# Performance work log

Hardware: AMD Instinct MI355X
Metric: run time of the kernel (lower is better)

The kernel has to match this reference:

```python
import jax, jax.numpy as jnp
import numpy as np

NODE_DIM, EDGE_DIM, HIDDEN = 64, 16, 128
B, N, E, EA = 4, 10000, 320000, 80000


def _lin(key, fan_in, fan_out):
    # xavier-uniform like torch init
    bound = (6.0 / (fan_in + fan_out)) ** 0.5
    w = jax.random.uniform(key, (fan_in, fan_out), jnp.float32, -bound, bound)
    b = jnp.zeros((fan_out,), jnp.float32)
    return w, b


def setup_inputs() -> dict:
    key = jax.random.key(0)
    ks = jax.random.split(key, 12)
    nodes = jax.random.normal(ks[0], (B, N, NODE_DIM), jnp.float32)
    edge_index = jax.random.randint(ks[1], (2, E), 0, N, jnp.int64)
    edge_attr = jax.random.normal(ks[2], (B, E, EDGE_DIM), jnp.float32)
    edge_type_mask = jax.random.randint(ks[3], (EA,), 0, E, jnp.int64)
    p = {}
    p['g1_mw1'], p['g1_mb1'] = _lin(ks[4], 2 * NODE_DIM + EDGE_DIM, HIDDEN)
    p['g1_mw2'], p['g1_mb2'] = _lin(ks[5], HIDDEN, HIDDEN)
    p['g1_uw'], p['g1_ub'] = _lin(ks[6], NODE_DIM + HIDDEN, HIDDEN)
    p['g2_mw1'], p['g2_mb1'] = _lin(ks[7], 2 * HIDDEN + EDGE_DIM, HIDDEN)
    p['g2_mw2'], p['g2_mb2'] = _lin(ks[8], HIDDEN, HIDDEN)
    p['g2_uw'], p['g2_ub'] = _lin(ks[9], HIDDEN + HIDDEN, HIDDEN)
    p['a_w1'], p['a_b1'] = _lin(ks[10], 2 * HIDDEN + EDGE_DIM, HIDDEN)
    p['a_w2'], p['a_b2'] = _lin(ks[11], HIDDEN, 2)
    return dict(nodes=nodes, edge_index=edge_index, edge_attr=edge_attr,
                edge_type_mask=edge_type_mask, **p)


def _gnn_layer(node_attr, edge_index, edge_attr, mw1, mb1, mw2, mb2, uw, ub):
    r, s = edge_index[0], edge_index[1]
    h_recv = node_attr[:, r, :]          # [B,E,D] gather
    h_sent = node_attr[:, s, :]
    msg_in = jnp.concatenate([h_recv, h_sent, edge_attr], axis=-1)
    msg = jax.nn.relu(msg_in @ mw1 + mb1) @ mw2 + mb2   # [B,E,H]
    Bn, Nn, _ = node_attr.shape
    agg = jnp.zeros((Bn, Nn, msg.shape[-1]), msg.dtype).at[:, r, :].add(msg)
    upd_in = jnp.concatenate([node_attr, agg], axis=-1)
    return jax.nn.relu(upd_in @ uw + ub)


def reference(nodes, edge_index, edge_attr, edge_type_mask,
              g1_mw1, g1_mb1, g1_mw2, g1_mb2, g1_uw, g1_ub,
              g2_mw1, g2_mb1, g2_mw2, g2_mb2, g2_uw, g2_ub,
              a_w1, a_b1, a_w2, a_b2):
    h = _gnn_layer(nodes, edge_index, edge_attr, g1_mw1, g1_mb1, g1_mw2, g1_mb2, g1_uw, g1_ub)
    h = _gnn_layer(h, edge_index, edge_attr, g2_mw1, g2_mb1, g2_mw2, g2_mb2, g2_uw, g2_ub)
    # actor head: gather active edges only
    r, s = edge_index[0], edge_index[1]
    ra, sa = r[edge_type_mask], s[edge_type_mask]
    h_recv_a = h[:, ra, :]
    h_sent_a = h[:, sa, :]
    e_a = edge_attr[:, edge_type_mask, :]
    x = jnp.concatenate([h_recv_a, h_sent_a, e_a], axis=-1)
    out = jax.nn.relu(x @ a_w1 + a_b1) @ a_w2 + a_b2     # [B,EA,2]
    out = out.reshape(out.shape[0], -1, 2, out.shape[2]).mean(axis=2)  # avg edge pairs
    mean = out[:, :, 0]
    log_std = jnp.clip(out[:, :, 1], -20.0, 2.0)
    std = jnp.exp(log_std)
    return mean, std
```

## Files before the change

### kernel.cpp

```cpp
#include <hip/hip_runtime.h>
#include <hip/hip_bf16.h>
#include <math.h>

constexpr int Bn  = 4;
constexpr int Nn  = 10000;
constexpr int En  = 320000;
constexpr int EAn = 80000;
constexpr int OUT_N = 2 * Bn * (EAn / 2);

__global__ __launch_bounds__(256) void fill_sentinel(float* out, float v) {
    const int i = blockIdx.x * 256 + threadIdx.x;
    if (i < OUT_N) out[i] = v;
}

__global__ __launch_bounds__(256) void decode_indices(const void* __restrict__ ei_raw,
                                                      const void* __restrict__ mask_raw,
                                                      int* __restrict__ ei32,
                                                      int* __restrict__ mask32) {
    __shared__ int is64;
    if (threadIdx.x == 0) {
        const long long* p = (const long long*)ei_raw;
        int ok = 1;
        for (int i = 0; i < 64; i++) {
            const long long v = p[i];
            if (v < 0 || v >= (long long)Nn) { ok = 0; break; }
        }
        is64 = ok;
    }
    __syncthreads();
    const int idx    = blockIdx.x * 256 + threadIdx.x;
    const int stride = gridDim.x * 256;
    if (is64) {
        for (int i = idx; i < 2 * En; i += stride)
            ei32[i] = (int)((const long long*)ei_raw)[i];
        for (int i = idx; i < EAn; i += stride)
            mask32[i] = (int)((const long long*)mask_raw)[i];
    } else {
        for (int i = idx; i < 2 * En; i += stride)
            ei32[i] = ((const int*)ei_raw)[i];
        for (int i = idx; i < EAn; i += stride)
            mask32[i] = ((const int*)mask_raw)[i];
    }
}

__global__ __launch_bounds__(256) void count_deg(const int* __restrict__ ei,
                                                 int* __restrict__ degi) {
    const int e = blockIdx.x * 256 + threadIdx.x;
    if (e < En) atomicAdd(&degi[ei[e]], 1);
}

__global__ __launch_bounds__(256) void scan_rowstart(const int* __restrict__ degi,
                                                     int* __restrict__ row_start) {
    __shared__ int buf[256];
    __shared__ int carry_s;
    const int tid = threadIdx.x;
    if (tid == 0) { carry_s = 0; row_start[0] = 0; }
    __syncthreads();
    for (int t = 0; t < 40; t++) {
        const int i = t * 256 + tid;
        buf[tid] = (i < Nn) ? degi[i] : 0;
        __syncthreads();
        for (int off = 1; off < 256; off <<= 1) {
            const int x = (tid >= off) ? buf[tid - off] : 0;
            __syncthreads();
            buf[tid] += x;
            __syncthreads();
        }
        const int base = carry_s;
        if (i < Nn) row_start[i + 1] = base + buf[tid];
        __syncthreads();
        if (tid == 255) carry_s = base + buf[255];
        __syncthreads();
    }
}

__global__ __launch_bounds__(256) void fill_csr(const int* __restrict__ ei,
                                                const int* __restrict__ row_start,
                                                int* __restrict__ cursor,
                                                unsigned int* __restrict__ rs_sorted,
                                                int* __restrict__ eid_sorted) {
    const int e = blockIdx.x * 256 + threadIdx.x;
    if (e < En) {
        const int r   = ei[e];
        const int s   = ei[En + e];
        const int pos = row_start[r] + atomicAdd(&cursor[r], 1);
        rs_sorted[pos]  = ((unsigned int)r << 16) | (unsigned int)s;
        eid_sorted[pos] = e;
    }
}

template <int KX>
__global__ __launch_bounds__(256) void precompute_P(const float* __restrict__ X,
                                                    const float* __restrict__ W,
                                                    float* __restrict__ P) {
    __shared__ float xs[16 * KX];
    const int m0  = blockIdx.x * 16;
    const int tid = threadIdx.x;

    for (int idx = tid * 4; idx < 16 * KX; idx += 1024)
        *(float4*)&xs[idx] = *(const float4*)&X[(size_t)m0 * KX + idx];
    __syncthreads();

    const int col  = tid;
    const int side = col >> 7;
    const int jj   = col & 127;
    const float* Wp = W + (size_t)(side * KX) * 128 + jj;

    float acc[16];
#pragma unroll
    for (int i = 0; i < 16; i++) acc[i] = 0.f;

    for (int k = 0; k < KX; k += 4) {
        const float w0 = Wp[(size_t)(k + 0) * 128];
        const float w1 = Wp[(size_t)(k + 1) * 128];
        const float w2 = Wp[(size_t)(k + 2) * 128];
        const float w3 = Wp[(size_t)(k + 3) * 128];
#pragma unroll
        for (int i = 0; i < 16; i++) {
            const float4 x = *(const float4*)&xs[i * KX + k];
            acc[i] += x.x * w0;
            acc[i] += x.y * w1;
            acc[i] += x.z * w2;
            acc[i] += x.w * w3;
        }
    }
#pragma unroll
    for (int i = 0; i < 16; i++) P[(size_t)(m0 + i) * 256 + col] = acc[i];
}

__global__ __launch_bounds__(256) void edge_scatter_sorted(const float* __restrict__ P,
                                                           const unsigned int* __restrict__ rs_sorted,
                                                           const int* __restrict__ eid_sorted,
                                                           const float* __restrict__ edge_attr,
                                                           const float* __restrict__ We,
                                                           const float* __restrict__ b1,
                                                           float* __restrict__ aggH) {
    __shared__ int   rc[32], sc[32], ec[32];
    __shared__ float eas[32 * 16];

    const int b   = blockIdx.y;
    const int e0  = blockIdx.x * 32;
    const int tid = threadIdx.x;

    if (tid < 32) {
        const unsigned int v = rs_sorted[e0 + tid];
        rc[tid] = (int)(v >> 16);
        sc[tid] = (int)(v & 0xffffu);
        ec[tid] = eid_sorted[e0 + tid];
    }
    __syncthreads();
    {
        const float* eab = edge_attr + (size_t)b * En * 16;
        if (tid < 128) {
            const int e = tid >> 2, k0 = (tid & 3) * 4;
            *(float4*)&eas[e * 16 + k0] = *(const float4*)&eab[(size_t)ec[e] * 16 + k0];
        }
    }
    __syncthreads();

    const int col  = tid & 127;
    const int half = tid >> 7;
    const int eb   = half * 16;

    float w[16];
#pragma unroll
    for (int k = 0; k < 16; k++) w[k] = We[k * 128 + col];
    const float b1c = b1[col];

    const float* Pb   = P + (size_t)b * Nn * 256;
    float*       aggb = aggH + (size_t)b * Nn * 128;

    float run  = 0.f;
    int   curR = rc[eb];
#pragma unroll 4
    for (int i = 0; i < 16; i++) {
        const int e = eb + i;
        const int r = rc[e];
        float a = b1c + Pb[(size_t)r * 256 + col]
                      + Pb[(size_t)sc[e] * 256 + 128 + col];
        const float4 e0v = *(const float4*)&eas[e * 16 + 0];
        const float4 e1v = *(const float4*)&eas[e * 16 + 4];
        const float4 e2v = *(const float4*)&eas[e * 16 + 8];
        const float4 e3v = *(const float4*)&eas[e * 16 + 12];
        a += e0v.x * w[0];  a += e0v.y * w[1];  a += e0v.z * w[2];  a += e0v.w * w[3];
        a += e1v.x * w[4];  a += e1v.y * w[5];  a += e1v.z * w[6];  a += e1v.w * w[7];
        a += e2v.x * w[8];  a += e2v.y * w[9];  a += e2v.z * w[10]; a += e2v.w * w[11];
        a += e3v.x * w[12]; a += e3v.y * w[13]; a += e3v.z * w[14]; a += e3v.w * w[15];
        if (r != curR) {
            atomicAdd(&aggb[(size_t)curR * 128 + col], run);
            run  = 0.f;
            curR = r;
        }
        run += fmaxf(a, 0.f);
    }
    atomicAdd(&aggb[(size_t)curR * 128 + col], run);
}

template <int KX>
__global__ __launch_bounds__(256) void fused_node(const float* __restrict__ X,
                                                  const float* __restrict__ aggH,
                                                  const float* __restrict__ W2,
                                                  const float* __restrict__ b2,
                                                  const int* __restrict__ row_start,
                                                  const float* __restrict__ uw,
                                                  const float* __restrict__ ub,
                                                  float* Hout) {
    __shared__ float ah[16 * 128];
    __shared__ float ag[16 * 128];
    __shared__ float xs[16 * KX];
    __shared__ float dg[16];

    const int m0  = blockIdx.x * 16;
    const int tid = threadIdx.x;

    if (tid < 16) {
        const int row = m0 + tid;
        const int nl  = row - (row / Nn) * Nn;
        dg[tid] = (float)(row_start[nl + 1] - row_start[nl]);
    }
    for (int idx = tid * 4; idx < 16 * 128; idx += 1024)
        *(float4*)&ah[idx] = *(const float4*)&aggH[(size_t)m0 * 128 + idx];
    for (int idx = tid * 4; idx < 16 * KX; idx += 1024)
        *(float4*)&xs[idx] = *(const float4*)&X[(size_t)m0 * KX + idx];
    __syncthreads();

    const int col  = tid & 127;
    const int half = tid >> 7;

    {
        const float b2c = b2[col];
        float acc[8];
#pragma unroll
        for (int i = 0; i < 8; i++) acc[i] = dg[half * 8 + i] * b2c;
        for (int k = 0; k < 128; k += 4) {
            const float w0 = W2[(k + 0) * 128 + col];
            const float w1 = W2[(k + 1) * 128 + col];
            const float w2v = W2[(k + 2) * 128 + col];
            const float w3 = W2[(k + 3) * 128 + col];
#pragma unroll
            for (int i = 0; i < 8; i++) {
                const float4 v = *(const float4*)&ah[(half * 8 + i) * 128 + k];
                acc[i] += v.x * w0;
                acc[i] += v.y * w1;
                acc[i] += v.z * w2v;
                acc[i] += v.w * w3;
            }
        }
#pragma unroll
        for (int i = 0; i < 8; i++) ag[(half * 8 + i) * 128 + col] = acc[i];
    }
    __syncthreads();

    float acc[8];
#pragma unroll
    for (int i = 0; i < 8; i++) acc[i] = ub[col];
    for (int k = 0; k < KX; k += 4) {
        const float w0 = uw[(size_t)(k + 0) * 128 + col];
        const float w1 = uw[(size_t)(k + 1) * 128 + col];
        const float w2v = uw[(size_t)(k + 2) * 128 + col];
        const float w3 = uw[(size_t)(k + 3) * 128 + col];
#pragma unroll
        for (int i = 0; i < 8; i++) {
            const float4 v = *(const float4*)&xs[(half * 8 + i) * KX + k];
            acc[i] += v.x * w0;
            acc[i] += v.y * w1;
            acc[i] += v.z * w2v;
            acc[i] += v.w * w3;
        }
    }
    for (int k = 0; k < 128; k += 4) {
        const float w0 = uw[(size_t)(KX + k + 0) * 128 + col];
        const float w1 = uw[(size_t)(KX + k + 1) * 128 + col];
        const float w2v = uw[(size_t)(KX + k + 2) * 128 + col];
        const float w3 = uw[(size_t)(KX + k + 3) * 128 + col];
#pragma unroll
        for (int i = 0; i < 8; i++) {
            const float4 v = *(const float4*)&ag[(half * 8 + i) * 128 + k];
            acc[i] += v.x * w0;
            acc[i] += v.y * w1;
            acc[i] += v.z * w2v;
            acc[i] += v.w * w3;
        }
    }
#pragma unroll
    for (int i = 0; i < 8; i++)
        Hout[(size_t)(m0 + half * 8 + i) * 128 + col] = fmaxf(acc[i], 0.f);
}

__global__ __launch_bounds__(256) void action_head_gather(const float* __restrict__ Pa,
                                                          const int* __restrict__ ei,
                                                          const float* __restrict__ edge_attr,
                                                          const int* __restrict__ mask,
                                                          const float* __restrict__ aWe,
                                                          const float* __restrict__ b1,
                                                          const float* __restrict__ w2,
                                                          const float* __restrict__ b2,
                                                          float* __restrict__ act) {
    __shared__ int   ridx[16];
    __shared__ int   sidx[16];
    __shared__ int   eidx[16];
    __shared__ float eas[16 * 17];
    __shared__ float wes[16 * 128];
    __shared__ float hid[16 * 129];

    const int b   = blockIdx.y;
    const int j0  = blockIdx.x * 16;
    const int tid = threadIdx.x;

    if (tid < 16) {
        const int e = mask[j0 + tid];
        eidx[tid]   = e;
        ridx[tid]   = ei[e];
        sidx[tid]   = ei[En + e];
    }
    for (int idx = tid * 4; idx < 16 * 128; idx += 1024)
        *(float4*)&wes[idx] = *(const float4*)&aWe[idx];
    __syncthreads();
    {
        const int e = tid >> 4, k = tid & 15;
        eas[e * 17 + k] = edge_attr[((size_t)b * En + eidx[e]) * 16 + k];
    }
    __syncthreads();

    const int col  = tid & 127;
    const int half = tid >> 7;
    const float bb = b1[col];
#pragma unroll
    for (int i = 0; i < 8; i++) {
        const int e = half * 8 + i;
        float a = bb + Pa[((size_t)b * Nn + ridx[e]) * 256 + col]
                     + Pa[((size_t)b * Nn + sidx[e]) * 256 + 128 + col];
#pragma unroll
        for (int k = 0; k < 16; k++) a += eas[e * 17 + k] * wes[k * 128 + col];
        hid[e * 129 + col] = fmaxf(a, 0.f);
    }
    __syncthreads();

    const int g    = tid >> 4;
    const int lane = tid & 15;
    float o0 = 0.f, o1 = 0.f;
#pragma unroll
    for (int k = lane; k < 128; k += 16) {
        const float hv = hid[g * 129 + k];
        o0 += hv * w2[k * 2 + 0];
        o1 += hv * w2[k * 2 + 1];
    }
#pragma unroll
    for (int m = 8; m >= 1; m >>= 1) {
        o0 += __shfl_xor(o0, m);
        o1 += __shfl_xor(o1, m);
    }
    if (lane == 0) {
        act[((size_t)b * EAn + j0 + g) * 2 + 0] = o0 + b2[0];
        act[((size_t)b * EAn + j0 + g) * 2 + 1] = o1 + b2[1];
    }
}

__global__ __launch_bounds__(256) void finalize(const float* __restrict__ act,
                                                float* __restrict__ out) {
    const int idx = blockIdx.x * 256 + threadIdx.x;
    constexpr int HALF = EAn / 2;
    if (idx >= Bn * HALF) return;
    const int b = idx / HALF, t = idx - b * HALF;
    const float* a = &act[((size_t)b * EAn + 2 * t) * 2];
    const float m = 0.5f * (a[0] + a[2]);
    float l       = 0.5f * (a[1] + a[3]);
    l = fminf(fmaxf(l, -20.f), 2.f);
    out[idx]             = m;
    out[Bn * HALF + idx] = expf(l);
}

extern "C" void kernel_launch(void* const* d_in, const int* in_sizes, int n_in,
                              void* d_out, int out_size, void* d_ws, size_t ws_size,
                              hipStream_t stream) {
    (void)out_size;

    static const long long want[20] = {
        (long long)Bn * Nn * 64, 2LL * En, (long long)Bn * En * 16, (long long)EAn,
        144 * 128, 128, 128 * 128, 128, 192 * 128, 128,
        272 * 128, 128, 128 * 128, 128, 256 * 128, 128,
        272 * 128, 128, 128 * 2, 2};
    bool sig_ok = (n_in == 20);
    if (sig_ok)
        for (int i = 0; i < 20; i++) sig_ok = sig_ok && (in_sizes[i] == want[i]);

    const size_t PF   = (size_t)Bn * Nn * 256;
    const size_t aggF = (size_t)Bn * Nn * 128;
    const size_t hF   = (size_t)Bn * Nn * 128;
    const size_t needWords = PF + aggF + hF + 2 * En + EAn + (Nn + 16) + En + En;
    const size_t needBytes = needWords * 4;

    const dim3 blk(256);
    if (!sig_ok) {
        fill_sentinel<<<(OUT_N + 255) / 256, blk, 0, stream>>>((float*)d_out, 5555.f);
        return;
    }
    if (ws_size < needBytes) {
        fill_sentinel<<<(OUT_N + 255) / 256, blk, 0, stream>>>((float*)d_out, 9999.f);
        return;
    }

    const float* nodes  = (const float*)d_in[0];
    const void*  ei_raw = d_in[1];
    const float* eattr  = (const float*)d_in[2];
    const void*  mk_raw = d_in[3];
    const float* g1_mw1 = (const float*)d_in[4];
    const float* g1_mb1 = (const float*)d_in[5];
    const float* g1_mw2 = (const float*)d_in[6];
    const float* g1_mb2 = (const float*)d_in[7];
    const float* g1_uw  = (const float*)d_in[8];
    const float* g1_ub  = (const float*)d_in[9];
    const float* g2_mw1 = (const float*)d_in[10];
    const float* g2_mb1 = (const float*)d_in[11];
    const float* g2_mw2 = (const float*)d_in[12];
    const float* g2_mb2 = (const float*)d_in[13];
    const float* g2_uw  = (const float*)d_in[14];
    const float* g2_ub  = (const float*)d_in[15];
    const float* a_w1   = (const float*)d_in[16];
    const float* a_b1   = (const float*)d_in[17];
    const float* a_w2   = (const float*)d_in[18];
    const float* a_b2   = (const float*)d_in[19];

    float*        P     = (float*)d_ws;
    float*        aggH  = P + PF;
    float*        h     = aggH + aggF;
    int*          ei32  = (int*)(h + hF);
    int*          mk32  = ei32 + 2 * En;
    int*          rowst = mk32 + EAn;
    unsigned int* rsS   = (unsigned int*)(rowst + (Nn + 16));
    int*          eidS  = (int*)(rsS + En);
    int*   degi = (int*)h;
    int*   cur  = degi + Nn;
    float* act  = h;

    const int  nbNodes = (Bn * Nn) / 16;
    const dim3 gEdge(En / 32, Bn);
    const dim3 gAct(EAn / 16, Bn);
    const size_t aggBytes = aggF * 4;

    decode_indices<<<2500, blk, 0, stream>>>(ei_raw, mk_raw, ei32, mk32);
    hipMemsetAsync(degi, 0, Nn * sizeof(int), stream);
    hipMemsetAsync(cur, 0, Nn * sizeof(int), stream);
    count_deg<<<En / 256, blk, 0, stream>>>(ei32, degi);
    scan_rowstart<<<1, blk, 0, stream>>>(degi, rowst);
    fill_csr<<<En / 256, blk, 0, stream>>>(ei32, rowst, cur, rsS, eidS);

    precompute_P<64><<<nbNodes, blk, 0, stream>>>(nodes, g1_mw1, P);
    hipMemsetAsync(aggH, 0, aggBytes, stream);
    edge_scatter_sorted<<<gEdge, blk, 0, stream>>>(P, rsS, eidS, eattr,
                                                   g1_mw1 + 128 * 128, g1_mb1, aggH);
    fused_node<64><<<nbNodes, blk, 0, stream>>>(nodes, aggH, g1_mw2, g1_mb2, rowst,
                                                g1_uw, g1_ub, h);

    precompute_P<128><<<nbNodes, blk, 0, stream>>>(h, g2_mw1, P);
    hipMemsetAsync(aggH, 0, aggBytes, stream);
    edge_scatter_sorted<<<gEdge, blk, 0, stream>>>(P, rsS, eidS, eattr,
                                                   g2_mw1 + 256 * 128, g2_mb1, aggH);
    fused_node<128><<<nbNodes, blk, 0, stream>>>(h, aggH, g2_mw2, g2_mb2, rowst,
                                                 g2_uw, g2_ub, h);

    precompute_P<128><<<nbNodes, blk, 0, stream>>>(h, a_w1, P);
    action_head_gather<<<gAct, blk, 0, stream>>>(P, ei32, eattr, mk32,
                                                 a_w1 + 256 * 128, a_b1,
                                                 a_w2, a_b2, act);
    finalize<<<(Bn * (EAn / 2) + 255) / 256, blk, 0, stream>>>(act, (float*)d_out);
}
```

Baseline: 840.7 us.

## Fuse next-layer projection into node update and fold finalize into action head

The node-update kernel now also computes the next stage's P projection (receiver and sender halves) from the freshly computed hidden state held in shared memory, and in layer 1 it zeroes the aggregation buffer itself. This removes the separate precompute_P launches, the h round-trip for layer 2, and the memsets. The action head now does the pair-averaging, clamp and exp itself, so the finalize kernel and its intermediate buffer go away. Smaller changes: the scan uses wavefront shuffles instead of a shared-memory Hillis-Steele loop, degree counters are zeroed inside decode, and the edge-attribute dot products are split into two accumulators. The fused node kernel does more work per block, which may raise register pressure. The layer-1 zeroing overwrites aggH rows the same block has just read, and relies on layer 2 reusing aggH only after the kernel finishes.

```diff
diff --git a/kernel.cpp b/kernel.cpp
--- a/kernel.cpp
+++ b/kernel.cpp
@@ -16,7 +16,9 @@
 __global__ __launch_bounds__(256) void decode_indices(const void* __restrict__ ei_raw,
                                                       const void* __restrict__ mask_raw,
                                                       int* __restrict__ ei32,
-                                                      int* __restrict__ mask32) {
+                                                      int* __restrict__ mask32,
+                                                      int* __restrict__ degi,
+                                                      int* __restrict__ cur) {
     __shared__ int is64;
     if (threadIdx.x == 0) {
         const long long* p = (const long long*)ei_raw;
@@ -41,6 +43,7 @@
         for (int i = idx; i < EAn; i += stride)
             mask32[i] = ((const int*)mask_raw)[i];
     }
+    for (int i = idx; i < Nn; i += stride) { degi[i] = 0; cur[i] = 0; }
 }
 
 __global__ __launch_bounds__(256) void count_deg(const int* __restrict__ ei,
@@ -51,25 +54,29 @@
 
 __global__ __launch_bounds__(256) void scan_rowstart(const int* __restrict__ degi,
                                                      int* __restrict__ row_start) {
-    __shared__ int buf[256];
+    __shared__ int wsum[4];
     __shared__ int carry_s;
-    const int tid = threadIdx.x;
+    const int tid  = threadIdx.x;
+    const int lane = tid & 63;
+    const int wv   = tid >> 6;
     if (tid == 0) { carry_s = 0; row_start[0] = 0; }
     __syncthreads();
     for (int t = 0; t < 40; t++) {
         const int i = t * 256 + tid;
-        buf[tid] = (i < Nn) ? degi[i] : 0;
+        int v = (i < Nn) ? degi[i] : 0;
+#pragma unroll
+        for (int off = 1; off < 64; off <<= 1) {
+            const int x = __shfl_up(v, off);
+            if (lane >= off) v += x;
+        }
+        if (lane == 63) wsum[wv] = v;
         __syncthreads();
-        for (int off = 1; off < 256; off <<= 1) {
-            const int x = (tid >= off) ? buf[tid - off] : 0;
-            __syncthreads();
-            buf[tid] += x;
-            __syncthreads();
-        }
+        int add = 0;
+        for (int w = 0; w < wv; w++) add += wsum[w];
         const int base = carry_s;
-        if (i < Nn) row_start[i + 1] = base + buf[tid];
+        if (i < Nn) row_start[i + 1] = base + add + v;
         __syncthreads();
-        if (tid == 255) carry_s = base + buf[255];
+        if (tid == 255) carry_s = base + add + v;
         __syncthreads();
     }
 }
@@ -176,35 +183,37 @@
     for (int i = 0; i < 16; i++) {
         const int e = eb + i;
         const int r = rc[e];
-        float a = b1c + Pb[(size_t)r * 256 + col]
-                      + Pb[(size_t)sc[e] * 256 + 128 + col];
+        float a0 = b1c + Pb[(size_t)r * 256 + col];
+        float a1 = Pb[(size_t)sc[e] * 256 + 128 + col];
         const float4 e0v = *(const float4*)&eas[e * 16 + 0];
         const float4 e1v = *(const float4*)&eas[e * 16 + 4];
         const float4 e2v = *(const float4*)&eas[e * 16 + 8];
         const float4 e3v = *(const float4*)&eas[e * 16 + 12];
-        a += e0v.x * w[0];  a += e0v.y * w[1];  a += e0v.z * w[2];  a += e0v.w * w[3];
-        a += e1v.x * w[4];  a += e1v.y * w[5];  a += e1v.z * w[6];  a += e1v.w * w[7];
-        a += e2v.x * w[8];  a += e2v.y * w[9];  a += e2v.z * w[10]; a += e2v.w * w[11];
-        a += e3v.x * w[12]; a += e3v.y * w[13]; a += e3v.z * w[14]; a += e3v.w * w[15];
+        a0 += e0v.x * w[0];  a1 += e0v.y * w[1];  a0 += e0v.z * w[2];  a1 += e0v.w * w[3];
+        a0 += e1v.x * w[4];  a1 += e1v.y * w[5];  a0 += e1v.z * w[6];  a1 += e1v.w * w[7];
+        a0 += e2v.x * w[8];  a1 += e2v.y * w[9];  a0 += e2v.z * w[10]; a1 += e2v.w * w[11];
+        a0 += e3v.x * w[12]; a1 += e3v.y * w[13]; a0 += e3v.z * w[14]; a1 += e3v.w * w[15];
         if (r != curR) {
             atomicAdd(&aggb[(size_t)curR * 128 + col], run);
             run  = 0.f;
             curR = r;
         }
-        run += fmaxf(a, 0.f);
+        run += fmaxf(a0 + a1, 0.f);
     }
     atomicAdd(&aggb[(size_t)curR * 128 + col], run);
 }
 
-template <int KX>
-__global__ __launch_bounds__(256) void fused_node(const float* __restrict__ X,
-                                                  const float* __restrict__ aggH,
-                                                  const float* __restrict__ W2,
-                                                  const float* __restrict__ b2,
-                                                  const int* __restrict__ row_start,
-                                                  const float* __restrict__ uw,
-                                                  const float* __restrict__ ub,
-                                                  float* Hout) {
+template <int KX, bool ZERO_AGG, bool WRITE_H>
+__global__ __launch_bounds__(256) void fused_node_p(const float* __restrict__ X,
+                                                    float* __restrict__ aggH,
+                                                    const float* __restrict__ W2,
+                                                    const float* __restrict__ b2,
+                                                    const int* __restrict__ row_start,
+                                                    const float* __restrict__ uw,
+                                                    const float* __restrict__ ub,
+                                                    const float* __restrict__ Wnext,
+                                                    float* __restrict__ Hout,
+                                                    float* __restrict__ Pout) {
     __shared__ float ah[16 * 128];
     __shared__ float ag[16 * 128];
     __shared__ float xs[16 * KX];
@@ -223,6 +232,12 @@
     for (int idx = tid * 4; idx < 16 * KX; idx += 1024)
         *(float4*)&xs[idx] = *(const float4*)&X[(size_t)m0 * KX + idx];
     __syncthreads();
+
+    if (ZERO_AGG) {
+        const float4 z = {0.f, 0.f, 0.f, 0.f};
+        for (int idx = tid * 4; idx < 16 * 128; idx += 1024)
+            *(float4*)&aggH[(size_t)m0 * 128 + idx] = z;
+    }
 
     const int col  = tid & 127;
     const int half = tid >> 7;
@@ -251,57 +266,91 @@
     }
     __syncthreads();
 
-    float acc[8];
-#pragma unroll
-    for (int i = 0; i < 8; i++) acc[i] = ub[col];
-    for (int k = 0; k < KX; k += 4) {
-        const float w0 = uw[(size_t)(k + 0) * 128 + col];
-        const float w1 = uw[(size_t)(k + 1) * 128 + col];
-        const float w2v = uw[(size_t)(k + 2) * 128 + col];
-        const float w3 = uw[(size_t)(k + 3) * 128 + col];
+    {
+        float acc[8];
+#pragma unroll
+        for (int i = 0; i < 8; i++) acc[i] = ub[col];
+        for (int k = 0; k < KX; k += 4) {
+            const float w0 = uw[(size_t)(k + 0) * 128 + col];
+            const float w1 = uw[(size_t)(k + 1) * 128 + col];
+            const float w2v = uw[(size_t)(k + 2) * 128 + col];
+            const float w3 = uw[(size_t)(k + 3) * 128 + col];
+#pragma unroll
+            for (int i = 0; i < 8; i++) {
+                const float4 v = *(const float4*)&xs[(half * 8 + i) * KX + k];
+                acc[i] += v.x * w0;
+                acc[i] += v.y * w1;
+                acc[i] += v.z * w2v;
+                acc[i] += v.w * w3;
+            }
+        }
+        for (int k = 0; k < 128; k += 4) {
+            const float w0 = uw[(size_t)(KX + k + 0) * 128 + col];
+            const float w1 = uw[(size_t)(KX + k + 1) * 128 + col];
+            const float w2v = uw[(size_t)(KX + k + 2) * 128 + col];
+            const float w3 = uw[(size_t)(KX + k + 3) * 128 + col];
+#pragma unroll
+            for (int i = 0; i < 8; i++) {
+                const float4 v = *(const float4*)&ag[(half * 8 + i) * 128 + k];
+                acc[i] += v.x * w0;
+                acc[i] += v.y * w1;
+                acc[i] += v.z * w2v;
+                acc[i] += v.w * w3;
+            }
+        }
 #pragma unroll
         for (int i = 0; i < 8; i++) {
-            const float4 v = *(const float4*)&xs[(half * 8 + i) * KX + k];
-            acc[i] += v.x * w0;
-            acc[i] += v.y * w1;
-            acc[i] += v.z * w2v;
-            acc[i] += v.w * w3;
-        }
-    }
-    for (int k = 0; k < 128; k += 4) {
-        const float w0 = uw[(size_t)(KX + k + 0) * 128 + col];
-        const float w1 = uw[(size_t)(KX + k + 1) * 128 + col];
-        const float w2v = uw[(size_t)(KX + k + 2) * 128 + col];
-        const float w3 = uw[(size_t)(KX + k + 3) * 128 + col];
-#pragma unroll
-        for (int i = 0; i < 8; i++) {
-            const float4 v = *(const float4*)&ag[(half * 8 + i) * 128 + k];
-            acc[i] += v.x * w0;
-            acc[i] += v.y * w1;
-            acc[i] += v.z * w2v;
-            acc[i] += v.w * w3;
-        }
-    }
-#pragma unroll
-    for (int i = 0; i < 8; i++)
-        Hout[(size_t)(m0 + half * 8 + i) * 128 + col] = fmaxf(acc[i], 0.f);
-}
-
-__global__ __launch_bounds__(256) void action_head_gather(const float* __restrict__ Pa,
-                                                          const int* __restrict__ ei,
-                                                          const float* __restrict__ edge_attr,
-                                                          const int* __restrict__ mask,
-                                                          const float* __restrict__ aWe,
-                                                          const float* __restrict__ b1,
-                                                          const float* __restrict__ w2,
-                                                          const float* __restrict__ b2,
-                                                          float* __restrict__ act) {
+            const float hv = fmaxf(acc[i], 0.f);
+            ah[(half * 8 + i) * 128 + col] = hv;
+            if (WRITE_H)
+                Hout[(size_t)(m0 + half * 8 + i) * 128 + col] = hv;
+        }
+    }
+    __syncthreads();
+
+    {
+        const int pcol = tid;
+        const int side = pcol >> 7;
+        const int jj   = pcol & 127;
+        const float* Wp = Wnext + (size_t)(side * 128) * 128 + jj;
+        float pacc[16];
+#pragma unroll
+        for (int i = 0; i < 16; i++) pacc[i] = 0.f;
+        for (int k = 0; k < 128; k += 4) {
+            const float w0 = Wp[(size_t)(k + 0) * 128];
+            const float w1 = Wp[(size_t)(k + 1) * 128];
+            const float w2v = Wp[(size_t)(k + 2) * 128];
+            const float w3 = Wp[(size_t)(k + 3) * 128];
+#pragma unroll
+            for (int i = 0; i < 16; i++) {
+                const float4 v = *(const float4*)&ah[i * 128 + k];
+                pacc[i] += v.x * w0;
+                pacc[i] += v.y * w1;
+                pacc[i] += v.z * w2v;
+                pacc[i] += v.w * w3;
+            }
+        }
+#pragma unroll
+        for (int i = 0; i < 16; i++)
+            Pout[(size_t)(m0 + i) * 256 + pcol] = pacc[i];
+    }
+}
+
+__global__ __launch_bounds__(256) void action_head_final(const float* __restrict__ Pa,
+                                                         const int* __restrict__ ei,
+                                                         const float* __restrict__ edge_attr,
+                                                         const int* __restrict__ mask,
+                                                         const float* __restrict__ aWe,
+                                                         const float* __restrict__ b1,
+                                                         const float* __restrict__ w2,
+                                                         const float* __restrict__ b2,
+                                                         float* __restrict__ out) {
     __shared__ int   ridx[16];
     __shared__ int   sidx[16];
     __shared__ int   eidx[16];
-    __shared__ float eas[16 * 17];
-    __shared__ float wes[16 * 128];
+    __shared__ float eas[16 * 16];
     __shared__ float hid[16 * 129];
+    __shared__ float o01[32];
 
     const int b   = blockIdx.y;
     const int j0  = blockIdx.x * 16;
@@ -313,26 +362,36 @@
         ridx[tid]   = ei[e];
         sidx[tid]   = ei[En + e];
     }
-    for (int idx = tid * 4; idx < 16 * 128; idx += 1024)
-        *(float4*)&wes[idx] = *(const float4*)&aWe[idx];
-    __syncthreads();
-    {
-        const int e = tid >> 4, k = tid & 15;
-        eas[e * 17 + k] = edge_attr[((size_t)b * En + eidx[e]) * 16 + k];
+    __syncthreads();
+    if (tid < 64) {
+        const float* eab = edge_attr + (size_t)b * En * 16;
+        const int e = tid >> 2, k0 = (tid & 3) * 4;
+        *(float4*)&eas[e * 16 + k0] = *(const float4*)&eab[(size_t)eidx[e] * 16 + k0];
     }
     __syncthreads();
 
     const int col  = tid & 127;
     const int half = tid >> 7;
-    const float bb = b1[col];
+    float w[16];
+#pragma unroll
+    for (int k = 0; k < 16; k++) w[k] = aWe[k * 128 + col];
+    const float b1c = b1[col];
+    const float* Pab = Pa + (size_t)b * Nn * 256;
+
 #pragma unroll
     for (int i = 0; i < 8; i++) {
         const int e = half * 8 + i;
-        float a = bb + Pa[((size_t)b * Nn + ridx[e]) * 256 + col]
-                     + Pa[((size_t)b * Nn + sidx[e]) * 256 + 128 + col];
-#pragma unroll
-        for (int k = 0; k < 16; k++) a += eas[e * 17 + k] * wes[k * 128 + col];
-        hid[e * 129 + col] = fmaxf(a, 0.f);
+        float a0 = b1c + Pab[(size_t)ridx[e] * 256 + col];
+        float a1 = Pab[(size_t)sidx[e] * 256 + 128 + col];
+        const float4 e0v = *(const float4*)&eas[e * 16 + 0];
+        const float4 e1v = *(const float4*)&eas[e * 16 + 4];
+        const float4 e2v = *(const float4*)&eas[e * 16 + 8];
+        const float4 e3v = *(const float4*)&eas[e * 16 + 12];
+        a0 += e0v.x * w[0];  a1 += e0v.y * w[1];  a0 += e0v.z * w[2];  a1 += e0v.w * w[3];
+        a0 += e1v.x * w[4];  a1 += e1v.y * w[5];  a0 += e1v.z * w[6];  a1 += e1v.w * w[7];
+        a0 += e2v.x * w[8];  a1 += e2v.y * w[9];  a0 += e2v.z * w[10]; a1 += e2v.w * w[11];
+        a0 += e3v.x * w[12]; a1 += e3v.y * w[13]; a0 += e3v.z * w[14]; a1 += e3v.w * w[15];
+        hid[e * 129 + col] = fmaxf(a0 + a1, 0.f);
     }
     __syncthreads();
 
@@ -351,23 +410,20 @@
         o1 += __shfl_xor(o1, m);
     }
     if (lane == 0) {
-        act[((size_t)b * EAn + j0 + g) * 2 + 0] = o0 + b2[0];
-        act[((size_t)b * EAn + j0 + g) * 2 + 1] = o1 + b2[1];
-    }
-}
-
-__global__ __launch_bounds__(256) void finalize(const float* __restrict__ act,
-                                                float* __restrict__ out) {
-    const int idx = blockIdx.x * 256 + threadIdx.x;
-    constexpr int HALF = EAn / 2;
-    if (idx >= Bn * HALF) return;
-    const int b = idx / HALF, t = idx - b * HALF;
-    const float* a = &act[((size_t)b * EAn + 2 * t) * 2];
-    const float m = 0.5f * (a[0] + a[2]);
-    float l       = 0.5f * (a[1] + a[3]);
-    l = fminf(fmaxf(l, -20.f), 2.f);
-    out[idx]             = m;
-    out[Bn * HALF + idx] = expf(l);
+        o01[g * 2 + 0] = o0 + b2[0];
+        o01[g * 2 + 1] = o1 + b2[1];
+    }
+    __syncthreads();
+
+    if (tid < 8) {
+        const float mean = 0.5f * (o01[4 * tid + 0] + o01[4 * tid + 2]);
+        float l          = 0.5f * (o01[4 * tid + 1] + o01[4 * tid + 3]);
+        l = fminf(fmaxf(l, -20.f), 2.f);
+        constexpr int HALF = EAn / 2;
+        const int idx = b * HALF + j0 / 2 + tid;
+        out[idx]             = mean;
+        out[Bn * HALF + idx] = expf(l);
+    }
 }
 
 extern "C" void kernel_launch(void* const* d_in, const int* in_sizes, int n_in,
@@ -431,16 +487,13 @@
     int*          eidS  = (int*)(rsS + En);
     int*   degi = (int*)h;
     int*   cur  = degi + Nn;
-    float* act  = h;
 
     const int  nbNodes = (Bn * Nn) / 16;
     const dim3 gEdge(En / 32, Bn);
     const dim3 gAct(EAn / 16, Bn);
     const size_t aggBytes = aggF * 4;
 
-    decode_indices<<<2500, blk, 0, stream>>>(ei_raw, mk_raw, ei32, mk32);
-    hipMemsetAsync(degi, 0, Nn * sizeof(int), stream);
-    hipMemsetAsync(cur, 0, Nn * sizeof(int), stream);
+    decode_indices<<<2500, blk, 0, stream>>>(ei_raw, mk_raw, ei32, mk32, degi, cur);
     count_deg<<<En / 256, blk, 0, stream>>>(ei32, degi);
     scan_rowstart<<<1, blk, 0, stream>>>(degi, rowst);
     fill_csr<<<En / 256, blk, 0, stream>>>(ei32, rowst, cur, rsS, eidS);
@@ -449,19 +502,15 @@
     hipMemsetAsync(aggH, 0, aggBytes, stream);
     edge_scatter_sorted<<<gEdge, blk, 0, stream>>>(P, rsS, eidS, eattr,
                                                    g1_mw1 + 128 * 128, g1_mb1, aggH);
-    fused_node<64><<<nbNodes, blk, 0, stream>>>(nodes, aggH, g1_mw2, g1_mb2, rowst,
-                                                g1_uw, g1_ub, h);
-
-    precompute_P<128><<<nbNodes, blk, 0, stream>>>(h, g2_mw1, P);
-    hipMemsetAsync(aggH, 0, aggBytes, stream);
+    fused_node_p<64, true, true><<<nbNodes, blk, 0, stream>>>(
+        nodes, aggH, g1_mw2, g1_mb2, rowst, g1_uw, g1_ub, g2_mw1, h, P);
+
     edge_scatter_sorted<<<gEdge, blk, 0, stream>>>(P, rsS, eidS, eattr,
                                                    g2_mw1 + 256 * 128, g2_mb1, aggH);
-    fused_node<128><<<nbNodes, blk, 0, stream>>>(h, aggH, g2_mw2, g2_mb2, rowst,
-                                                 g2_uw, g2_ub, h);
-
-    precompute_P<128><<<nbNodes, blk, 0, stream>>>(h, a_w1, P);
-    action_head_gather<<<gAct, blk, 0, stream>>>(P, ei32, eattr, mk32,
-                                                 a_w1 + 256 * 128, a_b1,
-                                                 a_w2, a_b2, act);
-    finalize<<<(Bn * (EAn / 2) + 255) / 256, blk, 0, stream>>>(act, (float*)d_out);
-}
+    fused_node_p<128, false, false><<<nbNodes, blk, 0, stream>>>(
+        h, aggH, g2_mw2, g2_mb2, rowst, g2_uw, g2_ub, a_w1, nullptr, P);
+
+    action_head_final<<<gAct, blk, 0, stream>>>(P, ei32, eattr, mk32,
+                                                a_w1 + 256 * 128, a_b1,
+                                                a_w2, a_b2, (float*)d_out);
+}
```

After: 759.5 us. 9.7% less time.
